# Kernel optimization log

Measured on AMD Instinct MI355X. Metric: run time of the kernel, lower is better.

The kernel has to match this reference:

```python
import jax, jax.numpy as jnp
import numpy as np

HIDDEN = 2048
NUM_HEADS = 16
NUM_KV_HEADS = 4
HEAD_DIM = HIDDEN // NUM_HEADS            # 128
Q_PER_KV = NUM_HEADS // NUM_KV_HEADS      # 4
GROUP_SIZE = (Q_PER_KV + 2) * HEAD_DIM    # 768
TOTAL_PROJ = NUM_KV_HEADS * GROUP_SIZE    # 3072
SEQ, BATCH = 2048, 2


def setup_inputs() -> dict:
    key = jax.random.key(0)
    k1, k2, k3 = jax.random.split(key, 3)
    x = jax.random.normal(k1, (SEQ, BATCH, HIDDEN), dtype=jnp.float32)
    weight_qkv = jax.random.normal(k2, (TOTAL_PROJ, HIDDEN), dtype=jnp.float32) * 0.02
    weight_proj = jax.random.normal(k3, (HIDDEN, NUM_HEADS * HEAD_DIM), dtype=jnp.float32) * 0.02
    return {"x": x, "weight_qkv": weight_qkv, "weight_proj": weight_proj}


def reference(x, weight_qkv, weight_proj):
    seq, batch, hidden = x.shape
    q_size = Q_PER_KV * HEAD_DIM

    # fused grouped QKV projection: [S*B, TOTAL_PROJ]
    qkv = x.reshape(-1, hidden) @ weight_qkv.T
    qkv = qkv.reshape(-1, NUM_KV_HEADS, GROUP_SIZE)
    q = qkv[:, :, :q_size].reshape(seq, batch, NUM_HEADS, HEAD_DIM)
    k = qkv[:, :, q_size:q_size + HEAD_DIM].reshape(seq, batch, NUM_KV_HEADS, HEAD_DIM)
    v = qkv[:, :, q_size + HEAD_DIM:].reshape(seq, batch, NUM_KV_HEADS, HEAD_DIM)

    # GQA: repeat_interleave kv heads to match q heads
    k = jnp.repeat(k, Q_PER_KV, axis=2)
    v = jnp.repeat(v, Q_PER_KV, axis=2)

    # [b, h, s, d]
    q = q.transpose(1, 2, 0, 3)
    k = k.transpose(1, 2, 0, 3)
    v = v.transpose(1, 2, 0, 3)

    scale = 1.0 / np.sqrt(HEAD_DIM)
    scores = jnp.einsum('bhqd,bhkd->bhqk', q, k) * scale
    causal = jnp.tril(jnp.ones((seq, seq), dtype=bool))
    scores = jnp.where(causal, scores, jnp.float32(-jnp.inf))
    probs = jax.nn.softmax(scores, axis=-1)
    attn = jnp.einsum('bhqk,bhkd->bhqd', probs, v)

    # back to [s, b, h*d] then output projection
    attn = attn.transpose(2, 0, 1, 3).reshape(seq * batch, NUM_HEADS * HEAD_DIM)
    out = attn @ weight_proj.T
    return out.reshape(seq, batch, hidden)
```

## Files before the change

### kernel.cpp

```cpp
#include <hip/hip_runtime.h>

#define SEQ 2048
#define BATCH 2
#define HIDDEN 2048
#define NHEADS 16
#define NKV 4
#define HD 128
#define GROUP 768
#define TPROJ 3072
#define NTOK (SEQ*BATCH)

typedef __attribute__((ext_vector_type(8))) __bf16 bf16x8;
typedef __attribute__((ext_vector_type(8))) unsigned short ushort8_t;
typedef __attribute__((ext_vector_type(4))) float f32x4;

union U8cast { ushort8_t u; bf16x8 b; };
__device__ inline bf16x8 as_bf(ushort8_t u) { U8cast c; c.u = u; return c.b; }

union Bf16U { __bf16 h; unsigned short u; };

__device__ inline unsigned short f2bf(float f) {
    unsigned int u = __float_as_uint(f);
    return (unsigned short)((u + 0x7FFFu + ((u >> 16) & 1u)) >> 16);
}

__device__ inline ushort8_t load8_f32_bf16(const float* __restrict__ p) {
    float4 v0 = *(const float4*)p;
    float4 v1 = *(const float4*)(p + 4);
    ushort8_t u;
    u[0] = f2bf(v0.x); u[1] = f2bf(v0.y); u[2] = f2bf(v0.z); u[3] = f2bf(v0.w);
    u[4] = f2bf(v1.x); u[5] = f2bf(v1.y); u[6] = f2bf(v1.z); u[7] = f2bf(v1.w);
    return u;
}

__device__ inline float exp2a(float x) {
    float r; asm("v_exp_f32 %0, %1" : "=v"(r) : "v"(x)); return r;
}

__device__ inline void gload_lds16(const unsigned short* g, unsigned short* l) {
    __builtin_amdgcn_global_load_lds(
        (const __attribute__((address_space(1))) void*)g,
        (__attribute__((address_space(3))) void*)l, 16, 0, 0);
}

#define CONV_N0 ((size_t)NTOK * HIDDEN)
#define CONV_N1 ((size_t)TPROJ * HIDDEN)
#define CONV_N2 ((size_t)HIDDEN * HIDDEN)
__global__ __launch_bounds__(256) void conv3_kernel(
    const float* __restrict__ x, const float* __restrict__ wq, const float* __restrict__ wp,
    unsigned short* __restrict__ xb, unsigned short* __restrict__ wqb, unsigned short* __restrict__ wpb)
{
    size_t i = (size_t)(blockIdx.x * 256 + threadIdx.x) * 8;
    if (i < CONV_N0) {
        *(ushort8_t*)(xb + i) = load8_f32_bf16(x + i);
    } else if (i < CONV_N0 + CONV_N1) {
        size_t j = i - CONV_N0;
        *(ushort8_t*)(wqb + j) = load8_f32_bf16(wq + j);
    } else {
        size_t j = i - CONV_N0 - CONV_N1;
        *(ushort8_t*)(wpb + j) = load8_f32_bf16(wp + j);
    }
}

template<bool OUT_BF16>
__global__ __launch_bounds__(512, 2) void gemm256_kernel(
    const unsigned short* __restrict__ A, const unsigned short* __restrict__ B,
    void* __restrict__ Cv, int M, int N, int K)
{
    __shared__ unsigned short lds[2][2][256 * 64];

    const int t = threadIdx.x, lane = t & 63, w = t >> 6;
    const int wm = w >> 2, wn = w & 3;
    const int l16 = lane & 15, lg = lane >> 4;

    const int cpx = (int)gridDim.x >> 3;
    const int wg  = ((int)blockIdx.x & 7) * cpx + ((int)blockIdx.x >> 3);
    const int nbn = N >> 8;
    const int m0 = (wg / nbn) << 8, n0 = (wg % nbn) << 8;
    const int NKT = K >> 6;

    const int srow = lane >> 3;
    const int scol = ((lane & 7) ^ srow) << 3;

    f32x4 acc[8][4] = {};

    auto stage = [&](const unsigned short* __restrict__ G, int g0, int kt, int op) {
        const int k0 = kt << 6;
        unsigned short* Ld = lds[kt & 1][op];
#pragma unroll
        for (int i = 0; i < 4; ++i) {
            const int r = w * 32 + i * 8;
            gload_lds16(G + (size_t)(g0 + r + srow) * K + k0 + scol, Ld + r * 64);
        }
    };

    stage(A, m0, 0, 0); stage(B, n0, 0, 1);
    stage(A, m0, 1, 0); stage(B, n0, 1, 1);

    for (int kt = 0; kt < NKT; ++kt) {
        const unsigned short* As_ = lds[kt & 1][0];
        const unsigned short* Bs_ = lds[kt & 1][1];

        if (kt < NKT - 1) asm volatile("s_waitcnt vmcnt(8)" ::: "memory");
        else              asm volatile("s_waitcnt vmcnt(0)" ::: "memory");
        __builtin_amdgcn_sched_barrier(0);
        __builtin_amdgcn_s_barrier();
        __builtin_amdgcn_sched_barrier(0);

        bf16x8 aR[8], b0R[4], b1R[4];

#pragma unroll
        for (int i = 0; i < 4; ++i)
#pragma unroll
            for (int s = 0; s < 2; ++s) {
                int row  = wm * 128 + i * 16 + l16;
                int slot = ((s << 2) | lg) ^ (l16 & 7);
                aR[i * 2 + s] = as_bf(*(const ushort8_t*)&As_[row * 64 + slot * 8]);
            }
#pragma unroll
        for (int j = 0; j < 2; ++j)
#pragma unroll
            for (int s = 0; s < 2; ++s) {
                int row  = wn * 64 + j * 16 + l16;
                int slot = ((s << 2) | lg) ^ (l16 & 7);
                b0R[j * 2 + s] = as_bf(*(const ushort8_t*)&Bs_[row * 64 + slot * 8]);
            }
        __builtin_amdgcn_s_setprio(1);
#pragma unroll
        for (int i = 0; i < 4; ++i)
#pragma unroll
            for (int j = 0; j < 2; ++j)
#pragma unroll
                for (int s = 0; s < 2; ++s)
                    acc[i][j] = __builtin_amdgcn_mfma_f32_16x16x32_bf16(aR[i*2+s], b0R[j*2+s], acc[i][j], 0, 0, 0);
        __builtin_amdgcn_s_setprio(0);

#pragma unroll
        for (int j = 0; j < 2; ++j)
#pragma unroll
            for (int s = 0; s < 2; ++s) {
                int row  = wn * 64 + 32 + j * 16 + l16;
                int slot = ((s << 2) | lg) ^ (l16 & 7);
                b1R[j * 2 + s] = as_bf(*(const ushort8_t*)&Bs_[row * 64 + slot * 8]);
            }
        __builtin_amdgcn_s_setprio(1);
#pragma unroll
        for (int i = 0; i < 4; ++i)
#pragma unroll
            for (int j = 0; j < 2; ++j)
#pragma unroll
                for (int s = 0; s < 2; ++s)
                    acc[i][2 + j] = __builtin_amdgcn_mfma_f32_16x16x32_bf16(aR[i*2+s], b1R[j*2+s], acc[i][2 + j], 0, 0, 0);
        __builtin_amdgcn_s_setprio(0);

        __builtin_amdgcn_sched_barrier(0);
        __builtin_amdgcn_s_barrier();
        __builtin_amdgcn_sched_barrier(0);
        if (kt + 2 < NKT) stage(B, n0, kt + 2, 1);
        __builtin_amdgcn_sched_barrier(0);

#pragma unroll
        for (int i = 0; i < 4; ++i)
#pragma unroll
            for (int s = 0; s < 2; ++s) {
                int row  = wm * 128 + 64 + i * 16 + l16;
                int slot = ((s << 2) | lg) ^ (l16 & 7);
                aR[i * 2 + s] = as_bf(*(const ushort8_t*)&As_[row * 64 + slot * 8]);
            }
        __builtin_amdgcn_s_setprio(1);
#pragma unroll
        for (int i = 0; i < 4; ++i)
#pragma unroll
            for (int j = 0; j < 2; ++j)
#pragma unroll
                for (int s = 0; s < 2; ++s)
                    acc[4 + i][2 + j] = __builtin_amdgcn_mfma_f32_16x16x32_bf16(aR[i*2+s], b1R[j*2+s], acc[4 + i][2 + j], 0, 0, 0);
        __builtin_amdgcn_s_setprio(0);

        __builtin_amdgcn_sched_barrier(0);
        __builtin_amdgcn_s_barrier();
        __builtin_amdgcn_sched_barrier(0);
        if (kt + 2 < NKT) stage(A, m0, kt + 2, 0);
        __builtin_amdgcn_sched_barrier(0);

        __builtin_amdgcn_s_setprio(1);
#pragma unroll
        for (int i = 0; i < 4; ++i)
#pragma unroll
            for (int j = 0; j < 2; ++j)
#pragma unroll
                for (int s = 0; s < 2; ++s)
                    acc[4 + i][j] = __builtin_amdgcn_mfma_f32_16x16x32_bf16(aR[i*2+s], b0R[j*2+s], acc[4 + i][j], 0, 0, 0);
        __builtin_amdgcn_s_setprio(0);
    }

#pragma unroll
    for (int ia = 0; ia < 8; ++ia)
#pragma unroll
        for (int jb = 0; jb < 4; ++jb)
#pragma unroll
            for (int r = 0; r < 4; ++r) {
                int row = m0 + wm * 128 + (ia >> 2) * 64 + (ia & 3) * 16 + lg * 4 + r;
                int col = n0 + wn * 64 + (jb >> 1) * 32 + (jb & 1) * 16 + l16;
                if (OUT_BF16)
                    ((unsigned short*)Cv)[(size_t)row * N + col] = f2bf(acc[ia][jb][r]);
                else
                    ((float*)Cv)[(size_t)row * N + col] = acc[ia][jb][r];
            }
}

__global__ __launch_bounds__(256) void vtrans_kernel(const unsigned short* __restrict__ qkv,
                                                     unsigned short* __restrict__ vT)
{
    const int t = threadIdx.x;
    const int s0 = blockIdx.x * 128 + (t & 15) * 8;
    const int bk = blockIdx.y;
    const int b_idx = bk >> 2;
    const int voff = (bk & 3) * GROUP + 640;
    const int d0 = (t >> 4) * 8;
    ushort8_t in[8];
#pragma unroll
    for (int j = 0; j < 8; ++j)
        in[j] = *(const ushort8_t*)(qkv + (size_t)((s0 + j) * BATCH + b_idx) * TPROJ + voff + d0);
#pragma unroll
    for (int dd = 0; dd < 8; ++dd) {
        ushort8_t ov;
#pragma unroll
        for (int j = 0; j < 8; ++j) ov[j] = in[j][dd];
        *(ushort8_t*)(vT + (size_t)(bk * HD + d0 + dd) * SEQ + s0) = ov;
    }
}

__global__ __launch_bounds__(256, 2) void attn_kernel(const unsigned short* __restrict__ qkv,
                                                      const unsigned short* __restrict__ vT,
                                                      unsigned short* __restrict__ attn_out)
{
    __shared__ unsigned short Ks[2][64][128];
    __shared__ unsigned short Vt[2][128][64];

    const int t = threadIdx.x, lane = t & 63, w = t >> 6;
    const int l16 = lane & 15, lg = lane >> 4;

    const int bid = (int)blockIdx.x;
    const int qt  = 127 - (bid >> 3);
    const int bk  = bid & 7;
    const int b_idx = bk >> 2;
    const int kvh   = bk & 3;
    const int qb0   = qt * 16;
    const int qoff  = kvh * GROUP + w * HD;
    const int koff  = kvh * GROUP + 512;
    const int vrow0 = (b_idx * NKV + kvh) * HD;
    const int h     = kvh * 4 + w;

    const float SCL2 = 0.08838834764831845f * 1.44269504f;
    const float THRU = 8.0f / SCL2;

    ushort8_t qf[4];
    {
        size_t qrow = (size_t)((qb0 + l16) * BATCH + b_idx) * TPROJ + qoff;
#pragma unroll
        for (int kc = 0; kc < 4; ++kc)
            qf[kc] = *(const ushort8_t*)(qkv + qrow + kc * 32 + lg * 8);
    }

    f32x4 o[8] = {};
    float mstate = -1e30f, lstate = 0.f, negm2 = 0.f;

    const int nIter = (qt >> 2) + 1;

    auto stageKV = [&](int it) {
        const int buf = it & 1;
        const int kv0 = it << 6;
#pragma unroll
        for (int i = 0; i < 4; ++i) {
            int rl = w * 16 + i * 4 + (lane >> 4);
            int pr = 32 * ((rl >> 4) & 1) + 8 * ((rl >> 2) & 3) + 4 * (rl >> 5) + (rl & 3);
            int g  = (lane & 15) ^ (rl & 7);
            gload_lds16(qkv + (size_t)((kv0 + pr) * BATCH + b_idx) * TPROJ + koff + g * 8,
                        &Ks[buf][w * 16 + i * 4][0]);
        }
#pragma unroll
        for (int i = 0; i < 4; ++i) {
            int rl = w * 32 + i * 8 + (lane >> 3);
            int g  = (lane & 7) ^ ((lane >> 3) & 7);
            gload_lds16(vT + (size_t)(vrow0 + rl) * SEQ + kv0 + g * 8,
                        &Vt[buf][w * 32 + i * 8][0]);
        }
    };

    stageKV(0);
    if (nIter > 1) stageKV(1);

    for (int it = 0; it < nIter; ++it) {
        const int buf = it & 1;
        const int kv0 = it * 64;

        if (it + 1 < nIter) asm volatile("s_waitcnt vmcnt(8)" ::: "memory");
        else                asm volatile("s_waitcnt vmcnt(0)" ::: "memory");
        __builtin_amdgcn_sched_barrier(0);
        __builtin_amdgcn_s_barrier();
        __builtin_amdgcn_sched_barrier(0);

        f32x4 s[4] = {};
        __builtin_amdgcn_s_setprio(1);
#pragma unroll
        for (int nf = 0; nf < 4; ++nf)
#pragma unroll
            for (int kc = 0; kc < 4; ++kc) {
                int phys = (kc * 4 + lg) ^ (l16 & 7);
                ushort8_t kb = *(const ushort8_t*)&Ks[buf][nf * 16 + l16][phys * 8];
                s[nf] = __builtin_amdgcn_mfma_f32_16x16x32_bf16(as_bf(kb), as_bf(qf[kc]), s[nf], 0, 0, 0);
            }
        __builtin_amdgcn_s_setprio(0);

        if (it == nIter - 1) {
            const int q_g = qb0 + l16;
#pragma unroll
            for (int nf = 0; nf < 4; ++nf)
#pragma unroll
                for (int r = 0; r < 4; ++r) {
                    int kv_g = kv0 + 32 * (nf & 1) + 8 * lg + 4 * (nf >> 1) + r;
                    if (kv_g > q_g) s[nf][r] = -1e30f;
                }
        }

        float a0 = fmaxf(fmaxf(s[0][0], s[0][1]), fmaxf(s[0][2], s[0][3]));
        float a1 = fmaxf(fmaxf(s[1][0], s[1][1]), fmaxf(s[1][2], s[1][3]));
        float a2 = fmaxf(fmaxf(s[2][0], s[2][1]), fmaxf(s[2][2], s[2][3]));
        float a3 = fmaxf(fmaxf(s[3][0], s[3][1]), fmaxf(s[3][2], s[3][3]));
        float rmax = fmaxf(fmaxf(a0, a1), fmaxf(a2, a3));
        rmax = fmaxf(rmax, __shfl_xor(rmax, 16));
        rmax = fmaxf(rmax, __shfl_xor(rmax, 32));

        if (!__all(rmax - mstate <= THRU)) {
            float mn = fmaxf(mstate, rmax);
            float corr = exp2a((mstate - mn) * SCL2);
            mstate = mn;
            negm2  = -mn * SCL2;
            lstate *= corr;
            float co[4];
#pragma unroll
            for (int r = 0; r < 4; ++r) co[r] = __shfl(corr, 4 * lg + r);
#pragma unroll
            for (int f = 0; f < 8; ++f)
#pragma unroll
                for (int r = 0; r < 4; ++r) o[f][r] *= co[r];
        }

        float p[4][4];
        float rs0 = 0.f, rs1 = 0.f;
#pragma unroll
        for (int nf = 0; nf < 4; ++nf)
#pragma unroll
            for (int r = 0; r < 4; ++r) {
                float pv = exp2a(fmaf(s[nf][r], SCL2, negm2));
                p[nf][r] = pv;
                if (nf < 2) rs0 += pv; else rs1 += pv;
            }
        float rsum = rs0 + rs1;
        rsum += __shfl_xor(rsum, 16);
        rsum += __shfl_xor(rsum, 32);
        lstate += rsum;

        ushort8_t paf[2];
#pragma unroll
        for (int c = 0; c < 2; ++c)
#pragma unroll
            for (int e = 0; e < 8; ++e) {
                Bf16U cv; cv.h = (__bf16)((e < 4) ? p[c][e] : p[2 + c][e - 4]);
                paf[c][e] = cv.u;
            }

        __builtin_amdgcn_s_setprio(1);
#pragma unroll
        for (int c = 0; c < 2; ++c)
#pragma unroll
            for (int f = 0; f < 8; ++f) {
                int phys = (c * 4 + lg) ^ (l16 & 7);
                ushort8_t vf = *(const ushort8_t*)&Vt[buf][l16 + 16 * f][phys * 8];
                o[f] = __builtin_amdgcn_mfma_f32_16x16x32_bf16(as_bf(paf[c]), as_bf(vf), o[f], 0, 0, 0);
            }
        __builtin_amdgcn_s_setprio(0);

        __builtin_amdgcn_sched_barrier(0);
        __builtin_amdgcn_s_barrier();
        __builtin_amdgcn_sched_barrier(0);
        if (it + 2 < nIter) stageKV(it + 2);
    }

    float li = 1.0f / lstate;
    float linv[4];
#pragma unroll
    for (int r = 0; r < 4; ++r) linv[r] = __shfl(li, 4 * lg + r);
#pragma unroll
    for (int f = 0; f < 8; ++f)
#pragma unroll
        for (int r = 0; r < 4; ++r) {
            int q_g = qb0 + lg * 4 + r;
            size_t row = (size_t)(q_g * BATCH + b_idx) * HIDDEN;
            attn_out[row + h * HD + 16 * f + l16] = f2bf(o[f][r] * linv[r]);
        }
}

extern "C" void kernel_launch(void* const* d_in, const int* in_sizes, int n_in,
                              void* d_out, int out_size, void* d_ws, size_t ws_size,
                              hipStream_t stream) {
    const float* x     = (const float*)d_in[0];
    const float* wqkv  = (const float*)d_in[1];
    const float* wproj = (const float*)d_in[2];
    float* out = (float*)d_out;

    unsigned short* qkv   = (unsigned short*)d_ws;
    unsigned short* attn  = qkv  + (size_t)NTOK * TPROJ;
    unsigned short* vT    = attn + (size_t)NTOK * HIDDEN;
    unsigned short* xb    = vT   + (size_t)BATCH * NKV * HD * SEQ;
    unsigned short* wqkvb = xb   + (size_t)NTOK * HIDDEN;
    unsigned short* wprojb= wqkvb+ (size_t)TPROJ * HIDDEN;

    conv3_kernel<<<dim3((unsigned)((CONV_N0 + CONV_N1 + CONV_N2) / 2048)), 256, 0, stream>>>(
        x, wqkv, wproj, xb, wqkvb, wprojb);

    gemm256_kernel<true><<<dim3((NTOK / 256) * (TPROJ / 256)), 512, 0, stream>>>(
        xb, wqkvb, (void*)qkv, NTOK, TPROJ, HIDDEN);

    vtrans_kernel<<<dim3(SEQ / 128, BATCH * NKV), 256, 0, stream>>>(qkv, vT);

    attn_kernel<<<dim3(1024), 256, 0, stream>>>(qkv, vT, attn);

    gemm256_kernel<false><<<dim3((NTOK / 256) * (HIDDEN / 256)), 512, 0, stream>>>(
        attn, wprojb, (void*)out, NTOK, HIDDEN, HIDDEN);
}
```

Before: 192.8 us.

## Replace double-buffered async LDS loads with register-staged single buffer for higher occupancy

```diff
diff --git a/kernel.cpp b/kernel.cpp
--- a/kernel.cpp
+++ b/kernel.cpp
@@ -231,12 +231,12 @@
     }
 }
 
-__global__ __launch_bounds__(256, 2) void attn_kernel(const unsigned short* __restrict__ qkv,
+__global__ __launch_bounds__(256, 4) void attn_kernel(const unsigned short* __restrict__ qkv,
                                                       const unsigned short* __restrict__ vT,
                                                       unsigned short* __restrict__ attn_out)
 {
-    __shared__ unsigned short Ks[2][64][128];
-    __shared__ unsigned short Vt[2][128][64];
+    __shared__ unsigned short Ks[64][128];
+    __shared__ unsigned short Vt[128][64];
 
     const int t = threadIdx.x, lane = t & 63, w = t >> 6;
     const int l16 = lane & 15, lg = lane >> 4;
@@ -268,35 +268,46 @@
 
     const int nIter = (qt >> 2) + 1;
 
-    auto stageKV = [&](int it) {
-        const int buf = it & 1;
+    const int rlK = w * 16 + (lane >> 4);
+    const int rlV = w * 32 + (lane >> 3);
+    ushort8_t kr[4], vr[4];
+
+    auto loadKV = [&](int it) {
         const int kv0 = it << 6;
 #pragma unroll
         for (int i = 0; i < 4; ++i) {
-            int rl = w * 16 + i * 4 + (lane >> 4);
+            int rl = rlK + i * 4;
             int pr = 32 * ((rl >> 4) & 1) + 8 * ((rl >> 2) & 3) + 4 * (rl >> 5) + (rl & 3);
-            int g  = (lane & 15) ^ (rl & 7);
-            gload_lds16(qkv + (size_t)((kv0 + pr) * BATCH + b_idx) * TPROJ + koff + g * 8,
-                        &Ks[buf][w * 16 + i * 4][0]);
+            kr[i] = *(const ushort8_t*)(qkv + (size_t)((kv0 + pr) * BATCH + b_idx) * TPROJ + koff + (lane & 15) * 8);
         }
 #pragma unroll
         for (int i = 0; i < 4; ++i) {
-            int rl = w * 32 + i * 8 + (lane >> 3);
-            int g  = (lane & 7) ^ ((lane >> 3) & 7);
-            gload_lds16(vT + (size_t)(vrow0 + rl) * SEQ + kv0 + g * 8,
-                        &Vt[buf][w * 32 + i * 8][0]);
+            int rl = rlV + i * 8;
+            vr[i] = *(const ushort8_t*)(vT + (size_t)(vrow0 + rl) * SEQ + kv0 + (lane & 7) * 8);
         }
     };
-
-    stageKV(0);
-    if (nIter > 1) stageKV(1);
+    auto writeKV = [&]() {
+#pragma unroll
+        for (int i = 0; i < 4; ++i) {
+            int rl = rlK + i * 4;
+            *(ushort8_t*)&Ks[rl][(((lane & 15) ^ (rl & 7))) * 8] = kr[i];
+        }
+#pragma unroll
+        for (int i = 0; i < 4; ++i) {
+            int rl = rlV + i * 8;
+            *(ushort8_t*)&Vt[rl][(((lane & 7) ^ (rl & 7))) * 8] = vr[i];
+        }
+    };
+
+    loadKV(0);
+    asm volatile("s_waitcnt vmcnt(0)" ::: "memory");
+    writeKV();
+    if (nIter > 1) loadKV(1);
 
     for (int it = 0; it < nIter; ++it) {
-        const int buf = it & 1;
         const int kv0 = it * 64;
 
-        if (it + 1 < nIter) asm volatile("s_waitcnt vmcnt(8)" ::: "memory");
-        else                asm volatile("s_waitcnt vmcnt(0)" ::: "memory");
+        asm volatile("s_waitcnt lgkmcnt(0)" ::: "memory");
         __builtin_amdgcn_sched_barrier(0);
         __builtin_amdgcn_s_barrier();
         __builtin_amdgcn_sched_barrier(0);
@@ -308,7 +319,7 @@
 #pragma unroll
             for (int kc = 0; kc < 4; ++kc) {
                 int phys = (kc * 4 + lg) ^ (l16 & 7);
-                ushort8_t kb = *(const ushort8_t*)&Ks[buf][nf * 16 + l16][phys * 8];
+                ushort8_t kb = *(const ushort8_t*)&Ks[nf * 16 + l16][phys * 8];
                 s[nf] = __builtin_amdgcn_mfma_f32_16x16x32_bf16(as_bf(kb), as_bf(qf[kc]), s[nf], 0, 0, 0);
             }
         __builtin_amdgcn_s_setprio(0);
@@ -347,14 +358,13 @@
                 for (int r = 0; r < 4; ++r) o[f][r] *= co[r];
         }
 
-        float p[4][4];
         float rs0 = 0.f, rs1 = 0.f;
 #pragma unroll
         for (int nf = 0; nf < 4; ++nf)
 #pragma unroll
             for (int r = 0; r < 4; ++r) {
                 float pv = exp2a(fmaf(s[nf][r], SCL2, negm2));
-                p[nf][r] = pv;
+                s[nf][r] = pv;
                 if (nf < 2) rs0 += pv; else rs1 += pv;
             }
         float rsum = rs0 + rs1;
@@ -367,7 +377,7 @@
         for (int c = 0; c < 2; ++c)
 #pragma unroll
             for (int e = 0; e < 8; ++e) {
-                Bf16U cv; cv.h = (__bf16)((e < 4) ? p[c][e] : p[2 + c][e - 4]);
+                Bf16U cv; cv.h = (__bf16)((e < 4) ? s[c][e] : s[2 + c][e - 4]);
                 paf[c][e] = cv.u;
             }
 
@@ -377,7 +387,7 @@
 #pragma unroll
             for (int f = 0; f < 8; ++f) {
                 int phys = (c * 4 + lg) ^ (l16 & 7);
-                ushort8_t vf = *(const ushort8_t*)&Vt[buf][l16 + 16 * f][phys * 8];
+                ushort8_t vf = *(const ushort8_t*)&Vt[l16 + 16 * f][phys * 8];
                 o[f] = __builtin_amdgcn_mfma_f32_16x16x32_bf16(as_bf(paf[c]), as_bf(vf), o[f], 0, 0, 0);
             }
         __builtin_amdgcn_s_setprio(0);
@@ -385,7 +395,11 @@
         __builtin_amdgcn_sched_barrier(0);
         __builtin_amdgcn_s_barrier();
         __builtin_amdgcn_sched_barrier(0);
-        if (it + 2 < nIter) stageKV(it + 2);
+        if (it + 1 < nIter) {
+            asm volatile("s_waitcnt vmcnt(0)" ::: "memory");
+            writeKV();
+            if (it + 2 < nIter) loadKV(it + 2);
+        }
     }
 
     float li = 1.0f / lstate;
```

Result: slower. 213.7 us (+10.9%).
